# Optimization experiments

Hardware: AMD Instinct MI355X
Metric: run time of the kernel (lower is better)

## Reference

```python
import jax, jax.numpy as jnp
import numpy as np

QMIN, QMAX = -128, 127  # get_quantized_range(8)


def setup_inputs() -> dict:
    key = jax.random.key(0)
    k1, k2, k3, k4 = jax.random.split(key, 4)
    N, IN, OUT = 8192, 4096, 4096
    x = jax.random.randint(k1, (N, IN), QMIN, QMAX + 1, dtype=jnp.int32).astype(jnp.int8)
    weight = jax.random.randint(k2, (OUT, IN), QMIN, QMAX + 1, dtype=jnp.int32).astype(jnp.int8)
    bias = jax.random.randint(k3, (OUT,), -1000, 1000, dtype=jnp.int32)
    weight_scale = jax.random.uniform(k4, (OUT,), dtype=jnp.float32, minval=1e-3, maxval=2e-2)
    return {
        "x": x,
        "weight": weight,
        "bias": bias,
        "weight_scale": weight_scale,
        "input_scale": 0.05,
        "output_scale": 0.1,
        "output_zero_point": -3,
    }


def reference(x, weight, bias, weight_scale, input_scale, output_scale, output_zero_point):
    # int8 GEMM accumulated in int32 (matches CPU path of the torch code)
    acc = jnp.matmul(x.astype(jnp.int32), weight.astype(jnp.int32).T) + bias[None, :]
    # fused per-channel dequant/requant epilogue
    scale = (input_scale * weight_scale / output_scale)[None, :]  # [1, OUT]
    out = acc.astype(jnp.float32) * scale + output_zero_point
    out = jnp.clip(jnp.round(out), QMIN, QMAX).astype(jnp.int8)
    return out
```

## Files before the change

kernel.cpp:

```cpp
#include <hip/hip_runtime.h>
#include <stdint.h>
#include <stddef.h>

typedef int v4i __attribute__((ext_vector_type(4)));

#define GLOAD16(gp, lp) __builtin_amdgcn_global_load_lds( \
    (const __attribute__((address_space(1))) void*)(gp),  \
    (__attribute__((address_space(3))) void*)(lp), 16, 0, 0)

#define PH_BAR()     __builtin_amdgcn_s_barrier()
#define WAIT_LGKM0() asm volatile("s_waitcnt lgkmcnt(0)" ::: "memory")
#define WAIT_VM(n)   asm volatile("s_waitcnt vmcnt(" #n ")" ::: "memory")
#define SCHED_FENCE() __builtin_amdgcn_sched_barrier(0)

static __device__ __forceinline__ int pack4(int a, int b, int c, int d) {
    return (a & 255) | ((b & 255) << 8) | ((c & 255) << 16) | (d << 24);
}

__global__ __launch_bounds__(256) void pack_kernel(const int* __restrict__ src,
                                                   v4i* __restrict__ dst, int n16) {
    int i = blockIdx.x * blockDim.x + threadIdx.x;
    if (i >= n16) return;
    const v4i* s = reinterpret_cast<const v4i*>(src) + (size_t)i * 4;
    v4i v0 = s[0], v1 = s[1], v2 = s[2], v3 = s[3];
    v4i r;
    r.x = pack4(v0.x, v0.y, v0.z, v0.w);
    r.y = pack4(v1.x, v1.y, v1.z, v1.w);
    r.z = pack4(v2.x, v2.y, v2.z, v2.w);
    r.w = pack4(v3.x, v3.y, v3.z, v3.w);
    dst[i] = r;
}

__global__ __launch_bounds__(512, 2) void gemm_q8_8ph(
    const char* __restrict__ Apk, const char* __restrict__ Bpk,
    const int* __restrict__ bias, const float* __restrict__ wscale,
    const float* __restrict__ is_p, const float* __restrict__ os_p,
    const int* __restrict__ zp_p,
    int* __restrict__ out, int K, int Ncols)
{
    __shared__ char lds[131072];

    const int tid  = threadIdx.x;
    const int wid  = tid >> 6;
    const int lane = tid & 63;
    const int l7 = lane & 7, l3 = lane >> 3;
    const int lo16 = lane & 15, hi = lane >> 4;

    int swz;
    {
        const int nwg = gridDim.x;
        const int q = nwg >> 3, r = nwg & 7;
        const int xcd = blockIdx.x & 7;
        const int base = (xcd < r) ? xcd * (q + 1) : r * (q + 1) + (xcd - r) * q;
        swz = base + (blockIdx.x >> 3);
    }
    const int nbc  = Ncols >> 8;
    const int brow = swz / nbc, bcol = swz % nbc;

    const int wr = wid >> 2, wc = wid & 3;

    const char* Ab = Apk + (size_t)(brow * 256 + wid * 8 + l3) * K + ((l7 ^ l3) << 4);
    const char* Bb = Bpk + (size_t)(bcol * 256 + wid * 8 + l3) * K + ((l7 ^ l3) << 4);

    const int colsw0 = (hi << 4) ^ (l7 << 4);
    const int colsw1 = colsw0 ^ 64;
    const int aRow = ((wr << 7) + lo16) << 7;
    const int bRow = ((wc << 6) + lo16) << 7;

    v4i acc[8][4];
#pragma unroll
    for (int m = 0; m < 8; ++m)
#pragma unroll
        for (int n = 0; n < 4; ++n)
            acc[m][n] = (v4i){0, 0, 0, 0};

    v4i af[4][2], bf[2][2], bf2[2][2];

    auto stage = [&](const char* gb, int ldsOp, int bufo, int h, int t) {
        const char* g = gb + (size_t)(h * 128) * K + ((size_t)t << 7);
        char* l = lds + (ldsOp + bufo + (h << 14) + (wid << 10));
        GLOAD16(g, l);
        GLOAD16(g + (size_t)64 * K, l + 8192);
    };
    auto ldA = [&](int bufo, int mh) {
#pragma unroll
        for (int m = 0; m < 4; ++m) {
            const int base = bufo + aRow + (mh << 13) + (m << 11);
            af[m][0] = *(const v4i*)(lds + base + colsw0);
            af[m][1] = *(const v4i*)(lds + base + colsw1);
        }
    };
    auto ldB = [&](v4i (&bx)[2][2], int bufo, int n0) {
#pragma unroll
        for (int n = 0; n < 2; ++n) {
            const int base = 65536 + bufo + bRow + ((n0 + n) << 11);
            bx[n][0] = *(const v4i*)(lds + base + colsw0);
            bx[n][1] = *(const v4i*)(lds + base + colsw1);
        }
    };

#define MFMA_Q(mo, bfx, no) do {                                                  \
    _Pragma("unroll") for (int m_ = 0; m_ < 4; ++m_)                              \
    _Pragma("unroll") for (int n_ = 0; n_ < 2; ++n_)                              \
    _Pragma("unroll") for (int s_ = 0; s_ < 2; ++s_)                              \
        acc[(mo) + m_][(no) + n_] = __builtin_amdgcn_mfma_i32_16x16x64_i8(        \
            af[m_][s_], bfx[n_][s_], acc[(mo) + m_][(no) + n_], 0, 0, 0);         \
} while (0)

    stage(Ab, 0,     0,     0, 0);  stage(Ab, 0,     0,     1, 0);
    stage(Bb, 65536, 0,     0, 0);  stage(Bb, 65536, 0,     1, 0);
    stage(Bb, 65536, 32768, 0, 1);  stage(Bb, 65536, 32768, 1, 1);
    WAIT_VM(4);
    PH_BAR();

    const int niter = K >> 8;
    for (int i = 0; i < niter; ++i) {
        SCHED_FENCE();
        const bool last = (i == niter - 1);
        const int tO1 = 2 * i + 1;
        const int tE  = 2 * i + 2, tO = 2 * i + 3;

        ldA(0, 0);
        ldB(bf, 0, 0);
        stage(Ab, 0, 32768, 0, tO1);
        PH_BAR(); WAIT_LGKM0();
        __builtin_amdgcn_s_setprio(1); MFMA_Q(0, bf, 0); __builtin_amdgcn_s_setprio(0);
        PH_BAR();
        ldB(bf2, 0, 2);
        stage(Ab, 0, 32768, 1, tO1);
        PH_BAR(); WAIT_LGKM0();
        __builtin_amdgcn_s_setprio(1); MFMA_Q(0, bf2, 2); __builtin_amdgcn_s_setprio(0);
        PH_BAR();
        ldA(0, 1);
        if (!last) stage(Bb, 65536, 0, 0, tE);
        PH_BAR(); WAIT_LGKM0();
        __builtin_amdgcn_s_setprio(1); MFMA_Q(4, bf, 0); __builtin_amdgcn_s_setprio(0);
        PH_BAR();
        if (!last) stage(Bb, 65536, 0, 1, tE);
        PH_BAR();
        __builtin_amdgcn_s_setprio(1); MFMA_Q(4, bf2, 2); __builtin_amdgcn_s_setprio(0);
        if (last) { WAIT_VM(0); } else { WAIT_VM(4); }
        PH_BAR();
        SCHED_FENCE();
        ldA(32768, 0);
        ldB(bf, 32768, 0);
        if (!last) stage(Ab, 0, 0, 0, tE);
        PH_BAR(); WAIT_LGKM0();
        __builtin_amdgcn_s_setprio(1); MFMA_Q(0, bf, 0); __builtin_amdgcn_s_setprio(0);
        PH_BAR();
        ldB(bf2, 32768, 2);
        if (!last) stage(Ab, 0, 0, 1, tE);
        PH_BAR(); WAIT_LGKM0();
        __builtin_amdgcn_s_setprio(1); MFMA_Q(0, bf2, 2); __builtin_amdgcn_s_setprio(0);
        PH_BAR();
        ldA(32768, 1);
        if (!last) stage(Bb, 65536, 32768, 0, tO);
        PH_BAR(); WAIT_LGKM0();
        __builtin_amdgcn_s_setprio(1); MFMA_Q(4, bf, 0); __builtin_amdgcn_s_setprio(0);
        PH_BAR();
        if (!last) stage(Bb, 65536, 32768, 1, tO);
        PH_BAR();
        __builtin_amdgcn_s_setprio(1); MFMA_Q(4, bf2, 2); __builtin_amdgcn_s_setprio(0);
        if (!last) { WAIT_VM(4); }
        PH_BAR();
    }
#undef MFMA_Q

    const float is = *is_p, os = *os_p;
    const float zp = (float)(*zp_p);
#pragma unroll
    for (int n = 0; n < 4; ++n) {
        const int col = (bcol << 8) + (wc << 6) + (n << 4) + lo16;
        const float sc = is * wscale[col] / os;
        const int   bv = bias[col];
#pragma unroll
        for (int m = 0; m < 8; ++m) {
            const int row0 = (brow << 8) + (wr << 7) + (m << 4) + (hi << 2);
#pragma unroll
            for (int j = 0; j < 4; ++j) {
                float f = (float)(acc[m][n][j] + bv) * sc + zp;
                f = rintf(f);
                f = fminf(fmaxf(f, -128.f), 127.f);
                out[(size_t)(row0 + j) * Ncols + col] = (int)f;
            }
        }
    }
}

template <bool PACKED>
__global__ __launch_bounds__(256) void gemm_q8(
    const void* __restrict__ Ain, const void* __restrict__ Bin,
    const int* __restrict__ bias, const float* __restrict__ wscale,
    const float* __restrict__ is_p, const float* __restrict__ os_p,
    const int* __restrict__ zp_p,
    int* __restrict__ out, int Nrows, int K, int Ncols)
{
    __shared__ char Al[128 * 64];
    __shared__ char Bl[128 * 64];

    const int tid  = threadIdx.x;
    const int wid  = tid >> 6;
    const int lane = tid & 63;

    const int nbc = Ncols / 128;
    int swz = blockIdx.x;
    if ((gridDim.x & 7) == 0) {
        const int cpx = gridDim.x >> 3;
        swz = (blockIdx.x & 7) * cpx + (blockIdx.x >> 3);
    }
    const int brow = swz / nbc;
    const int bcol = swz % nbc;
    const int wr = wid >> 1, wc = wid & 1;

    v4i acc[4][4];
#pragma unroll
    for (int m = 0; m < 4; ++m)
#pragma unroll
        for (int n = 0; n < 4; ++n)
            acc[m][n] = (v4i){0, 0, 0, 0};

    const char* Ag = nullptr;
    const char* Bg = nullptr;
    if (PACKED) {
        Ag = (const char*)Ain + (size_t)(brow * 128 + wid * 32 + (lane >> 2)) * K + (lane & 3) * 16;
        Bg = (const char*)Bin + (size_t)(bcol * 128 + wid * 32 + (lane >> 2)) * K + (lane & 3) * 16;
    }
    char* aldst = Al + wid * 2048;
    char* bldst = Bl + wid * 2048;

    const int lo16 = lane & 15, hi = lane >> 4;
    const int aoff0 = (wr * 64 + lo16) * 64 + hi * 16;
    const int boff0 = (wc * 64 + lo16) * 64 + hi * 16;

    for (int k0 = 0; k0 < K; k0 += 64) {
        if (PACKED) {
            GLOAD16(Ag + k0,          aldst);
            GLOAD16(Ag + 16 * K + k0, aldst + 1024);
            GLOAD16(Bg + k0,          bldst);
            GLOAD16(Bg + 16 * K + k0, bldst + 1024);
        } else {
            const int row = tid >> 1, half = tid & 1;
            const int* sA = (const int*)Ain + (size_t)(brow * 128 + row) * K + k0 + half * 32;
            const int* sB = (const int*)Bin + (size_t)(bcol * 128 + row) * K + k0 + half * 32;
            int pa[8], pb[8];
#pragma unroll
            for (int j = 0; j < 8; ++j) {
                v4i va = reinterpret_cast<const v4i*>(sA)[j];
                v4i vb = reinterpret_cast<const v4i*>(sB)[j];
                pa[j] = pack4(va.x, va.y, va.z, va.w);
                pb[j] = pack4(vb.x, vb.y, vb.z, vb.w);
            }
            v4i* da = (v4i*)&Al[row * 64 + half * 32];
            da[0] = (v4i){pa[0], pa[1], pa[2], pa[3]};
            da[1] = (v4i){pa[4], pa[5], pa[6], pa[7]};
            v4i* db = (v4i*)&Bl[row * 64 + half * 32];
            db[0] = (v4i){pb[0], pb[1], pb[2], pb[3]};
            db[1] = (v4i){pb[4], pb[5], pb[6], pb[7]};
        }
        __syncthreads();

        v4i af[4], bfr[4];
#pragma unroll
        for (int m = 0; m < 4; ++m)
            af[m] = *(const v4i*)&Al[aoff0 + m * 16 * 64];
#pragma unroll
        for (int n = 0; n < 4; ++n)
            bfr[n] = *(const v4i*)&Bl[boff0 + n * 16 * 64];
#pragma unroll
        for (int m = 0; m < 4; ++m)
#pragma unroll
            for (int n = 0; n < 4; ++n)
                acc[m][n] = __builtin_amdgcn_mfma_i32_16x16x64_i8(af[m], bfr[n], acc[m][n], 0, 0, 0);

        __syncthreads();
    }

    const float is = *is_p;
    const float os = *os_p;
    const float zp = (float)(*zp_p);
#pragma unroll
    for (int n = 0; n < 4; ++n) {
        const int col = bcol * 128 + wc * 64 + n * 16 + lo16;
        const float sc = is * wscale[col] / os;
        const int   bv = bias[col];
#pragma unroll
        for (int m = 0; m < 4; ++m) {
            const int row0 = brow * 128 + wr * 64 + m * 16 + hi * 4;
#pragma unroll
            for (int j = 0; j < 4; ++j) {
                float f = (float)(acc[m][n][j] + bv) * sc + zp;
                f = rintf(f);
                f = fminf(fmaxf(f, -128.f), 127.f);
                out[(size_t)(row0 + j) * Ncols + col] = (int)f;
            }
        }
    }
}

extern "C" void kernel_launch(void* const* d_in, const int* in_sizes, int n_in,
                              void* d_out, int out_size, void* d_ws, size_t ws_size,
                              hipStream_t stream) {
    const int*   x32    = (const int*)d_in[0];
    const int*   w32    = (const int*)d_in[1];
    const int*   bias   = (const int*)d_in[2];
    const float* wscale = (const float*)d_in[3];
    const float* isp    = (const float*)d_in[4];
    const float* osp    = (const float*)d_in[5];
    const int*   zpp    = (const int*)d_in[6];
    int* out = (int*)d_out;

    const int OUT = in_sizes[2];
    const int K   = in_sizes[1] / OUT;
    const int Nr  = in_sizes[0] / K;

    const size_t need = (size_t)Nr * K + (size_t)OUT * K;

    if (ws_size >= need) {
        char* xpk = (char*)d_ws;
        char* wpk = xpk + (size_t)Nr * K;
        const int nx16 = (Nr * K) / 16;
        const int nw16 = (OUT * K) / 16;
        pack_kernel<<<(nx16 + 255) / 256, 256, 0, stream>>>(x32, (v4i*)xpk, nx16);
        pack_kernel<<<(nw16 + 255) / 256, 256, 0, stream>>>(w32, (v4i*)wpk, nw16);
        if ((Nr & 255) == 0 && (OUT & 255) == 0 && (K & 255) == 0) {
            const int grid8 = (Nr / 256) * (OUT / 256);
            gemm_q8_8ph<<<grid8, 512, 0, stream>>>(xpk, wpk, bias, wscale, isp, osp, zpp,
                                                   out, K, OUT);
        } else {
            const int grid = (Nr / 128) * (OUT / 128);
            gemm_q8<true><<<grid, 256, 0, stream>>>(xpk, wpk, bias, wscale, isp, osp, zpp,
                                                    out, Nr, K, OUT);
        }
    } else {
        const int grid = (Nr / 128) * (OUT / 128);
        gemm_q8<false><<<grid, 256, 0, stream>>>(x32, w32, bias, wscale, isp, osp, zpp,
                                                 out, Nr, K, OUT);
    }
}
```

Before: 187.1 us.

## Prefetch B fragments across phases, peel last iteration, fuse pack kernels

The main loop now loads the first B fragment before the loop and prefetches the next B fragment during the previous phase's MFMAs. The final iteration is peeled out so the steady-state loop has no `last` conditionals, and the vmcnt waits are retuned. The two int32-to-int8 pack launches are merged into one kernel, and the epilogue is reordered so scale and bias are hoisted and stores are grouped per row. The K guard is tightened to multiples of 512, so other K values take the fallback kernel. The aim is to hide LDS read latency and cut launch and branch overhead.

```diff
diff --git a/kernel.cpp b/kernel.cpp
--- a/kernel.cpp
+++ b/kernel.cpp
@@ -12,15 +12,19 @@
 #define WAIT_LGKM0() asm volatile("s_waitcnt lgkmcnt(0)" ::: "memory")
 #define WAIT_VM(n)   asm volatile("s_waitcnt vmcnt(" #n ")" ::: "memory")
 #define SCHED_FENCE() __builtin_amdgcn_sched_barrier(0)
+#define PRIO1() __builtin_amdgcn_s_setprio(1)
+#define PRIO0() __builtin_amdgcn_s_setprio(0)
 
 static __device__ __forceinline__ int pack4(int a, int b, int c, int d) {
     return (a & 255) | ((b & 255) << 8) | ((c & 255) << 16) | (d << 24);
 }
 
-__global__ __launch_bounds__(256) void pack_kernel(const int* __restrict__ src,
-                                                   v4i* __restrict__ dst, int n16) {
+__global__ __launch_bounds__(256) void pack2_kernel(const int* __restrict__ srcA, v4i* __restrict__ dstA, int nA,
+                                                    const int* __restrict__ srcB, v4i* __restrict__ dstB, int nB) {
     int i = blockIdx.x * blockDim.x + threadIdx.x;
-    if (i >= n16) return;
+    const int* src; v4i* dst;
+    if (i < nA) { src = srcA; dst = dstA; }
+    else { i -= nA; if (i >= nB) return; src = srcB; dst = dstB; }
     const v4i* s = reinterpret_cast<const v4i*>(src) + (size_t)i * 4;
     v4i v0 = s[0], v1 = s[1], v2 = s[2], v3 = s[3];
     v4i r;
@@ -112,76 +116,119 @@
     stage(Bb, 65536, 32768, 0, 1);  stage(Bb, 65536, 32768, 1, 1);
     WAIT_VM(4);
     PH_BAR();
+    ldB(bf, 0, 0);
 
     const int niter = K >> 8;
-    for (int i = 0; i < niter; ++i) {
+    for (int i = 0; i < niter - 1; ++i) {
         SCHED_FENCE();
-        const bool last = (i == niter - 1);
-        const int tO1 = 2 * i + 1;
-        const int tE  = 2 * i + 2, tO = 2 * i + 3;
+        const int tO1 = 2 * i + 1, tE = 2 * i + 2, tO = 2 * i + 3;
 
         ldA(0, 0);
-        ldB(bf, 0, 0);
         stage(Ab, 0, 32768, 0, tO1);
         PH_BAR(); WAIT_LGKM0();
-        __builtin_amdgcn_s_setprio(1); MFMA_Q(0, bf, 0); __builtin_amdgcn_s_setprio(0);
+        PRIO1(); MFMA_Q(0, bf, 0); PRIO0();
         PH_BAR();
         ldB(bf2, 0, 2);
         stage(Ab, 0, 32768, 1, tO1);
         PH_BAR(); WAIT_LGKM0();
-        __builtin_amdgcn_s_setprio(1); MFMA_Q(0, bf2, 2); __builtin_amdgcn_s_setprio(0);
+        PRIO1(); MFMA_Q(0, bf2, 2); PRIO0();
         PH_BAR();
         ldA(0, 1);
-        if (!last) stage(Bb, 65536, 0, 0, tE);
-        PH_BAR(); WAIT_LGKM0();
-        __builtin_amdgcn_s_setprio(1); MFMA_Q(4, bf, 0); __builtin_amdgcn_s_setprio(0);
-        PH_BAR();
-        if (!last) stage(Bb, 65536, 0, 1, tE);
-        PH_BAR();
-        __builtin_amdgcn_s_setprio(1); MFMA_Q(4, bf2, 2); __builtin_amdgcn_s_setprio(0);
-        if (last) { WAIT_VM(0); } else { WAIT_VM(4); }
+        stage(Bb, 65536, 0, 0, tE);
+        PH_BAR(); WAIT_LGKM0();
+        PRIO1(); MFMA_Q(4, bf, 0); PRIO0();
+        WAIT_VM(6);
+        PH_BAR();
+        ldB(bf, 32768, 0);
+        stage(Bb, 65536, 0, 1, tE);
+        PH_BAR();
+        PRIO1(); MFMA_Q(4, bf2, 2); PRIO0();
+        WAIT_VM(4);
         PH_BAR();
         SCHED_FENCE();
         ldA(32768, 0);
+        stage(Ab, 0, 0, 0, tE);
+        PH_BAR(); WAIT_LGKM0();
+        PRIO1(); MFMA_Q(0, bf, 0); PRIO0();
+        PH_BAR();
+        ldB(bf2, 32768, 2);
+        stage(Ab, 0, 0, 1, tE);
+        PH_BAR(); WAIT_LGKM0();
+        PRIO1(); MFMA_Q(0, bf2, 2); PRIO0();
+        PH_BAR();
+        ldA(32768, 1);
+        stage(Bb, 65536, 32768, 0, tO);
+        PH_BAR(); WAIT_LGKM0();
+        PRIO1(); MFMA_Q(4, bf, 0); PRIO0();
+        WAIT_VM(6);
+        PH_BAR();
+        ldB(bf, 0, 0);
+        stage(Bb, 65536, 32768, 1, tO);
+        PH_BAR();
+        PRIO1(); MFMA_Q(4, bf2, 2); PRIO0();
+        WAIT_VM(4);
+        PH_BAR();
+    }
+
+    {
+        SCHED_FENCE();
+        const int tL = 2 * niter - 1;
+        ldA(0, 0);
+        stage(Ab, 0, 32768, 0, tL);
+        PH_BAR(); WAIT_LGKM0();
+        PRIO1(); MFMA_Q(0, bf, 0); PRIO0();
+        PH_BAR();
+        ldB(bf2, 0, 2);
+        stage(Ab, 0, 32768, 1, tL);
+        PH_BAR(); WAIT_LGKM0();
+        PRIO1(); MFMA_Q(0, bf2, 2); PRIO0();
+        PH_BAR();
+        ldA(0, 1);
+        PH_BAR(); WAIT_LGKM0();
+        PRIO1(); MFMA_Q(4, bf, 0); PRIO0();
+        WAIT_VM(0);
+        PH_BAR();
         ldB(bf, 32768, 0);
-        if (!last) stage(Ab, 0, 0, 0, tE);
-        PH_BAR(); WAIT_LGKM0();
-        __builtin_amdgcn_s_setprio(1); MFMA_Q(0, bf, 0); __builtin_amdgcn_s_setprio(0);
+        PH_BAR();
+        PRIO1(); MFMA_Q(4, bf2, 2); PRIO0();
+        PH_BAR();
+        ldA(32768, 0);
+        PH_BAR(); WAIT_LGKM0();
+        PRIO1(); MFMA_Q(0, bf, 0); PRIO0();
         PH_BAR();
         ldB(bf2, 32768, 2);
-        if (!last) stage(Ab, 0, 0, 1, tE);
-        PH_BAR(); WAIT_LGKM0();
-        __builtin_amdgcn_s_setprio(1); MFMA_Q(0, bf2, 2); __builtin_amdgcn_s_setprio(0);
+        PH_BAR(); WAIT_LGKM0();
+        PRIO1(); MFMA_Q(0, bf2, 2); PRIO0();
         PH_BAR();
         ldA(32768, 1);
-        if (!last) stage(Bb, 65536, 32768, 0, tO);
-        PH_BAR(); WAIT_LGKM0();
-        __builtin_amdgcn_s_setprio(1); MFMA_Q(4, bf, 0); __builtin_amdgcn_s_setprio(0);
-        PH_BAR();
-        if (!last) stage(Bb, 65536, 32768, 1, tO);
-        PH_BAR();
-        __builtin_amdgcn_s_setprio(1); MFMA_Q(4, bf2, 2); __builtin_amdgcn_s_setprio(0);
-        if (!last) { WAIT_VM(4); }
-        PH_BAR();
+        PH_BAR(); WAIT_LGKM0();
+        PRIO1(); MFMA_Q(4, bf, 0); PRIO0();
+        PH_BAR();
+        PRIO1(); MFMA_Q(4, bf2, 2); PRIO0();
     }
 #undef MFMA_Q
 
     const float is = *is_p, os = *os_p;
     const float zp = (float)(*zp_p);
+    const int colb = (bcol << 8) + (wc << 6) + lo16;
+    float sc[4]; int bv[4];
 #pragma unroll
     for (int n = 0; n < 4; ++n) {
-        const int col = (bcol << 8) + (wc << 6) + (n << 4) + lo16;
-        const float sc = is * wscale[col] / os;
-        const int   bv = bias[col];
-#pragma unroll
-        for (int m = 0; m < 8; ++m) {
-            const int row0 = (brow << 8) + (wr << 7) + (m << 4) + (hi << 2);
-#pragma unroll
-            for (int j = 0; j < 4; ++j) {
-                float f = (float)(acc[m][n][j] + bv) * sc + zp;
+        sc[n] = is * wscale[colb + (n << 4)] / os;
+        bv[n] = bias[colb + (n << 4)];
+    }
+#pragma unroll
+    for (int m = 0; m < 8; ++m) {
+#pragma unroll
+        for (int j = 0; j < 4; ++j) {
+            const int row = (brow << 8) + (wr << 7) + (m << 4) + (hi << 2) + j;
+            int* op = out + (size_t)row * Ncols + colb;
+#pragma unroll
+            for (int n = 0; n < 4; ++n) {
+                float f = (float)(acc[m][n][j] + bv[n]) * sc[n] + zp;
                 f = rintf(f);
                 f = fminf(fmaxf(f, -128.f), 127.f);
-                out[(size_t)(row0 + j) * Ncols + col] = (int)f;
+                op[n << 4] = (int)f;
             }
         }
     }
@@ -320,9 +367,9 @@
         char* wpk = xpk + (size_t)Nr * K;
         const int nx16 = (Nr * K) / 16;
         const int nw16 = (OUT * K) / 16;
-        pack_kernel<<<(nx16 + 255) / 256, 256, 0, stream>>>(x32, (v4i*)xpk, nx16);
-        pack_kernel<<<(nw16 + 255) / 256, 256, 0, stream>>>(w32, (v4i*)wpk, nw16);
-        if ((Nr & 255) == 0 && (OUT & 255) == 0 && (K & 255) == 0) {
+        pack2_kernel<<<(nx16 + nw16 + 255) / 256, 256, 0, stream>>>(
+            x32, (v4i*)xpk, nx16, w32, (v4i*)wpk, nw16);
+        if ((Nr & 255) == 0 && (OUT & 255) == 0 && (K & 511) == 0) {
             const int grid8 = (Nr / 256) * (OUT / 256);
             gemm_q8_8ph<<<grid8, 512, 0, stream>>>(xpk, wpk, bias, wscale, isp, osp, zpp,
                                                    out, K, OUT);
```

New measurement: 176.8 us. 5.5% less time.
